# Kernel tuning notes

Hardware: AMD Instinct MI355X
Metric: run time of the kernel (lower is better)

The kernel has to match this reference:

```python
import jax, jax.numpy as jnp
import numpy as np

B, S, H, DH = 4, 1024, 8, 64
D = H * DH
CLIP_K = 5
NUM_RPR = 2 * CLIP_K + 1  # 11


def setup_inputs() -> dict:
    key = jax.random.key(0)
    ks = jax.random.split(key, 12)
    w_scale = 0.01  # truncated_normal stddev approx
    inp = {
        'q': jax.random.normal(ks[0], (B, S, D), jnp.float32),
        'k': jax.random.normal(ks[1], (B, S, D), jnp.float32),
        'v': jax.random.normal(ks[2], (B, S, D), jnp.float32),
        'rpr_matrix': jax.random.randint(ks[3], (S, S), 0, NUM_RPR, jnp.int32),
        'wq_kernel': jax.random.normal(ks[4], (D, D), jnp.float32) * w_scale,
        'wq_bias': jnp.zeros((D,), jnp.float32),
        'wk_kernel': jax.random.normal(ks[5], (D, D), jnp.float32) * w_scale,
        'wk_bias': jnp.zeros((D,), jnp.float32),
        'wv_kernel': jax.random.normal(ks[6], (D, D), jnp.float32) * w_scale,
        'wv_bias': jnp.zeros((D,), jnp.float32),
        'krpr': jax.random.normal(ks[7], (NUM_RPR, DH), jnp.float32),
    }
    return inp


def reference(q, k, v, rpr_matrix, wq_kernel, wq_bias, wk_kernel, wk_bias,
              wv_kernel, wv_bias, krpr):
    b, s, d = q.shape
    dh = krpr.shape[-1]
    h = d // dh

    def proj(x, w, bias):
        # [B,S,D] -> [B,H,S,DH]
        y = x.reshape(-1, d) @ w + bias
        return y.reshape(b, s, h, dh).transpose(0, 2, 1, 3)

    qh = proj(q, wq_kernel, wq_bias)
    kh = proj(k, wk_kernel, wk_bias)
    vh = proj(v, wv_kernel, wv_bias)

    # standard QK^T scores
    scores = jnp.einsum('bhqd,bhkd->bhqk', qh, kh)
    # RPR key bias: gather per-relative-position key embeddings (note: original
    # code uses krpr for BOTH the key-side and value-side RPR; vrpr is unused)
    alpha = krpr[rpr_matrix]  # [Sq, Sk, DH]
    scores = scores + jnp.einsum('bhqd,qkd->bhqk', qh, alpha)
    scores = scores / jnp.sqrt(jnp.float32(dh))

    probs = jax.nn.softmax(scores, axis=-1)

    ctx = jnp.einsum('bhqk,bhkd->bhqd', probs, vh)
    ctx = ctx + jnp.einsum('bhqk,qkd->bhqd', probs, alpha)

    # [B,H,S,DH] -> [B,S,D]
    return ctx.transpose(0, 2, 1, 3).reshape(b, s, d)
```

## Files before the change

### kernel.cpp

```cpp
#include <hip/hip_runtime.h>

typedef unsigned short u16;
typedef unsigned int u32;
typedef __attribute__((ext_vector_type(8))) short short8;
typedef __attribute__((ext_vector_type(4))) float f32x4;
typedef _Float16 f16x2 __attribute__((ext_vector_type(2)));

__device__ __forceinline__ float bf2f(u16 v) {
  return __uint_as_float(((u32)v) << 16);
}
__device__ __forceinline__ u16 f2bf(float f) {
  u32 u = __float_as_uint(f);
  return (u16)((u + 0x7fffu + ((u >> 16) & 1u)) >> 16);
}
__device__ __forceinline__ u32 pk2(float lo, float hi) {
  return (u32)f2bf(lo) | ((u32)f2bf(hi) << 16);
}

__device__ __forceinline__ float ld1in(const void* p, size_t i, bool f32) {
  return f32 ? ((const float*)p)[i] : bf2f(((const u16*)p)[i]);
}
__device__ __forceinline__ float4 ld4in(const void* p, size_t i, bool f32) {
  if (f32) return *(const float4*)((const float*)p + i);
  ushort4 u = *(const ushort4*)((const u16*)p + i);
  return make_float4(bf2f(u.x), bf2f(u.y), bf2f(u.z), bf2f(u.w));
}

__device__ __forceinline__ uint4 ld8ws_pk(const u16* p, size_t i) {
  return *(const uint4*)(p + i);
}


__global__ void rpr_detect_kernel(const u16* __restrict__ q, int* __restrict__ flag) {
  __shared__ int cnt4[4];
  int t = threadIdx.x, c = 0;
  for (int i = t; i < 8192; i += 256) {
    unsigned e = (q[i] >> 7) & 0xff;
    c += (e >= 0xC0) ? 1 : 0;
  }
#pragma unroll
  for (int off = 1; off < 64; off <<= 1) c += __shfl_xor(c, off);
  if ((t & 63) == 0) cnt4[t >> 6] = c;
  __syncthreads();
  if (t == 0) *flag = (cnt4[0] + cnt4[1] + cnt4[2] + cnt4[3] > 128) ? 1 : 0;
}

template <typename WT>
__global__ __launch_bounds__(256, 2) void rpr_proj_mfma(
    const void* __restrict__ xq, const void* __restrict__ xk, const void* __restrict__ xv,
    const void* __restrict__ wqp, const void* __restrict__ wkp, const void* __restrict__ wvp,
    const void* __restrict__ bqp, const void* __restrict__ bkp, const void* __restrict__ bvp,
    WT* __restrict__ ws, const int* __restrict__ flagp) {
  const bool f32 = (*flagp != 0);
  const int z = blockIdx.z;
  const void* __restrict__ X = (z == 0) ? xq : (z == 1) ? xk : xv;
  const void* __restrict__ W = (z == 0) ? wqp : (z == 1) ? wkp : wvp;
  const void* __restrict__ Bb = (z == 0) ? bqp : (z == 1) ? bkp : bvp;
  WT* __restrict__ O = ws + (size_t)z * (4096u * 512u);

  __shared__ u32 as32[2][64][20];
  __shared__ u32 bs32[2][64][20];

  const int t = threadIdx.x;
  const int wvi = t >> 6, lane = t & 63;
  const int quad = lane >> 4, col = lane & 15;
  const int m0 = blockIdx.y * 64, n0 = blockIdx.x * 64;
  const int am = t >> 2, akc = t & 3;
  const int bkx = t & 15, bnx = (t >> 4) * 4;

  f32x4 acc[4] = {{0.f, 0.f, 0.f, 0.f}, {0.f, 0.f, 0.f, 0.f},
                  {0.f, 0.f, 0.f, 0.f}, {0.f, 0.f, 0.f, 0.f}};

  auto loadA = [&](int k0, uint4& ra) {
    if (!f32) {
      ra = *(const uint4*)((const u16*)X + (size_t)(m0 + am) * 512 + k0 + akc * 8);
    } else {
      const float* xf = (const float*)X + (size_t)(m0 + am) * 512 + k0 + akc * 8;
      float4 a = *(const float4*)xf, b = *(const float4*)(xf + 4);
      ra.x = pk2(a.x, a.y); ra.y = pk2(a.z, a.w);
      ra.z = pk2(b.x, b.y); ra.w = pk2(b.z, b.w);
    }
  };
  auto loadB = [&](int k0, uint4& rb) {
    if (!f32) {
      const u16* w0 = (const u16*)W + (size_t)(k0 + 2 * bkx) * 512 + n0 + bnx;
      ushort4 r0 = *(const ushort4*)w0;
      ushort4 r1 = *(const ushort4*)(w0 + 512);
      rb.x = (u32)r0.x | ((u32)r1.x << 16);
      rb.y = (u32)r0.y | ((u32)r1.y << 16);
      rb.z = (u32)r0.z | ((u32)r1.z << 16);
      rb.w = (u32)r0.w | ((u32)r1.w << 16);
    } else {
      float4 r0 = ld4in(W, (size_t)(k0 + 2 * bkx) * 512 + n0 + bnx, true);
      float4 r1 = ld4in(W, (size_t)(k0 + 2 * bkx + 1) * 512 + n0 + bnx, true);
      rb.x = pk2(r0.x, r1.x);
      rb.y = pk2(r0.y, r1.y);
      rb.z = pk2(r0.z, r1.z);
      rb.w = pk2(r0.w, r1.w);
    }
  };

  {
    uint4 ra, rb;
    loadA(0, ra);
    loadB(0, rb);
    *(uint4*)&as32[0][am][akc * 4] = ra;
    bs32[0][bnx + 0][bkx] = rb.x;
    bs32[0][bnx + 1][bkx] = rb.y;
    bs32[0][bnx + 2][bkx] = rb.z;
    bs32[0][bnx + 3][bkx] = rb.w;
  }
  __syncthreads();

  for (int it = 0; it < 16; ++it) {
    const int cur = it & 1;
    uint4 ra, rb;
    if (it < 15) {
      loadA((it + 1) * 32, ra);
      loadB((it + 1) * 32, rb);
    }
    short8 aF = *(const short8*)((const u16*)&as32[cur][wvi * 16 + col][0] + quad * 8);
#pragma unroll
    for (int c = 0; c < 4; ++c) {
      short8 bF = *(const short8*)((const u16*)&bs32[cur][c * 16 + col][0] + quad * 8);
      acc[c] = __builtin_amdgcn_mfma_f32_16x16x32_bf16(aF, bF, acc[c], 0, 0, 0);
    }
    if (it < 15) {
      *(uint4*)&as32[1 - cur][am][akc * 4] = ra;
      bs32[1 - cur][bnx + 0][bkx] = rb.x;
      bs32[1 - cur][bnx + 1][bkx] = rb.y;
      bs32[1 - cur][bnx + 2][bkx] = rb.z;
      bs32[1 - cur][bnx + 3][bkx] = rb.w;
    }
    __syncthreads();
  }

  const int h = blockIdx.x;
#pragma unroll
  for (int c = 0; c < 4; ++c) {
    float bias = ld1in(Bb, (size_t)(n0 + c * 16 + col), f32);
#pragma unroll
    for (int reg = 0; reg < 4; ++reg) {
      int m = m0 + wvi * 16 + quad * 4 + reg;
      int bb = m >> 10, s = m & 1023;
      O[((size_t)((bb * 8 + h) * 1024 + s)) * 64 + c * 16 + col] =
          f2bf(acc[c][reg] + bias);
    }
  }
}

template <typename WT>
__global__ __launch_bounds__(256, 2) void rpr_attn_mfma(
    const WT* __restrict__ qkv, const int* __restrict__ rpr,
    const void* __restrict__ krpr, void* __restrict__ out,
    const int* __restrict__ flagp) {
  const bool f32 = (*flagp != 0);
  const int bh = blockIdx.y, q0 = blockIdx.x * 64;
  const int b = bh >> 3, h = bh & 7;
  const WT* __restrict__ qh = qkv + (size_t)bh * 65536;
  const WT* __restrict__ kh = qkv + (size_t)(32 + bh) * 65536;
  const WT* __restrict__ vh = qkv + (size_t)(64 + bh) * 65536;

  __shared__ alignas(16) u16 qps[64][72];
  __shared__ u16 ks[2][64][72];
  __shared__ u32 vs32[2][64][36];
  __shared__ float krl[11][64];
  __shared__ float qrpr[64][12];

  const int t = threadIdx.x;
  const int wvi = t >> 6, lane = t & 63;
  const int quad = lane >> 4, col = lane & 15;
  const int sr = t >> 2, sc4 = (t & 3) * 16;
  const int kp = t & 31, dg = (t >> 5) * 8;
  const int swk = (((t & 3) + sr) & 3) * 16;
  const int fo0 = ((quad + 2 * (col & 3)) & 7) * 8;
  const int fo1 = fo0 ^ 32;
  const int vq = kp >> 2, vr = kp & 3;

  u16* __restrict__ psw = &qps[0][0] + wvi * (16 * 72);
  const int row0 = wvi * 16 + quad * 4;

  for (int i = t; i < 704; i += 256)
    krl[i >> 6][i & 63] = f32 ? ((const float*)krpr)[i] : bf2f(((const u16*)krpr)[i]);
  {
    size_t base = (size_t)(q0 + sr) * 64 + sc4;
    *(uint4*)&qps[sr][sc4] = ld8ws_pk(qh, base);
    *(uint4*)&qps[sr][sc4 + 8] = ld8ws_pk(qh, base + 8);
  }
  {
    size_t kb = (size_t)sr * 64 + sc4;
    *(uint4*)&ks[0][sr][swk] = ld8ws_pk(kh, kb);
    *(uint4*)&ks[0][sr][swk + 8] = ld8ws_pk(kh, kb + 8);
    size_t vb = (size_t)(2 * kp) * 64 + dg;
    uint4 va = ld8ws_pk(vh, vb), vbb = ld8ws_pk(vh, vb + 64);
    vs32[0][dg + 0][((vq + 0) & 7) * 4 + vr] = (va.x & 0xffffu) | (vbb.x << 16);
    vs32[0][dg + 1][((vq + 2) & 7) * 4 + vr] = (va.x >> 16) | (vbb.x & 0xffff0000u);
    vs32[0][dg + 2][((vq + 4) & 7) * 4 + vr] = (va.y & 0xffffu) | (vbb.y << 16);
    vs32[0][dg + 3][((vq + 6) & 7) * 4 + vr] = (va.y >> 16) | (vbb.y & 0xffff0000u);
    vs32[0][dg + 4][((vq + 0) & 7) * 4 + vr] = (va.z & 0xffffu) | (vbb.z << 16);
    vs32[0][dg + 5][((vq + 2) & 7) * 4 + vr] = (va.z >> 16) | (vbb.z & 0xffff0000u);
    vs32[0][dg + 6][((vq + 4) & 7) * 4 + vr] = (va.w & 0xffffu) | (vbb.w << 16);
    vs32[0][dg + 7][((vq + 6) & 7) * 4 + vr] = (va.w >> 16) | (vbb.w & 0xffff0000u);
  }
  int rid[4][4];
  {
    const int* rbase = rpr + (size_t)(q0 + row0) * 1024 + col;
#pragma unroll
    for (int reg = 0; reg < 4; ++reg)
#pragma unroll
      for (int c = 0; c < 4; ++c) rid[c][reg] = rbase[reg * 1024 + c * 16];
  }
  __syncthreads();
  {
    const float SC = 0.18033688011112042f;
    int r = t >> 2, rb = t & 3;
    float d0 = 0.f, d1 = 0.f, d2 = 0.f;
    for (int d = 0; d < 64; ++d) {
      float qv = bf2f(qps[r][d]);
      d0 = fmaf(qv, krl[rb][d], d0);
      d1 = fmaf(qv, krl[rb + 4][d], d1);
      if (rb < 3) d2 = fmaf(qv, krl[rb + 8][d], d2);
    }
    qrpr[r][rb] = d0 * SC;
    qrpr[r][rb + 4] = d1 * SC;
    if (rb < 3) qrpr[r][rb + 8] = d2 * SC;
  }
  short8 qA0, qA1;
  {
    const u16* qrow = &qps[wvi * 16 + col][0];
    qA0 = *(const short8*)(qrow + quad * 8);
    qA1 = *(const short8*)(qrow + 32 + quad * 8);
  }
  __syncthreads();

  float bins[4][11] = {};
  f32x4 ctx[4] = {{0.f, 0.f, 0.f, 0.f}, {0.f, 0.f, 0.f, 0.f},
                  {0.f, 0.f, 0.f, 0.f}, {0.f, 0.f, 0.f, 0.f}};

  for (int kt = 0; kt < 16; ++kt) {
    const int cur = kt & 1;
    uint4 pk0, pk1, pva, pvb;
    int ridn[4][4];
    if (kt < 15) {
      size_t kb = (size_t)((kt + 1) * 64 + sr) * 64 + sc4;
      pk0 = ld8ws_pk(kh, kb);
      pk1 = ld8ws_pk(kh, kb + 8);
      size_t vb = (size_t)((kt + 1) * 64 + 2 * kp) * 64 + dg;
      pva = ld8ws_pk(vh, vb);
      pvb = ld8ws_pk(vh, vb + 64);
      const int* rbase = rpr + (size_t)(q0 + row0) * 1024 + (kt + 1) * 64 + col;
#pragma unroll
      for (int reg = 0; reg < 4; ++reg)
#pragma unroll
        for (int c = 0; c < 4; ++c) ridn[c][reg] = rbase[reg * 1024 + c * 16];
    }
    f32x4 sc[4];
#pragma unroll
    for (int c = 0; c < 4; ++c) {
      const u16* kb = &ks[cur][c * 16 + col][0];
      short8 kB0 = *(const short8*)(kb + fo0);
      short8 kB1 = *(const short8*)(kb + fo1);
      f32x4 a = {0.f, 0.f, 0.f, 0.f};
      a = __builtin_amdgcn_mfma_f32_16x16x32_bf16(qA0, kB0, a, 0, 0, 0);
      a = __builtin_amdgcn_mfma_f32_16x16x32_bf16(qA1, kB1, a, 0, 0, 0);
      sc[c] = a;
    }
#pragma unroll
    for (int reg = 0; reg < 4; ++reg) {
      const int row = row0 + reg;
      float p4[4];
#pragma unroll
      for (int c = 0; c < 4; ++c) {
        float x = fmaf(sc[c][reg], 0.18033688011112042f, qrpr[row][rid[c][reg]]);
        float pe;
        asm("v_exp_f32 %0, %1" : "=v"(pe) : "v"(x));
        p4[c] = pe;
      }
      f16x2 ph01 = __builtin_bit_cast(f16x2, __builtin_amdgcn_cvt_pkrtz(p4[0], p4[1]));
      f16x2 ph23 = __builtin_bit_cast(f16x2, __builtin_amdgcn_cvt_pkrtz(p4[2], p4[3]));
      u32 m01 = (1u << (u32)rid[0][reg]) | (0x10000u << (u32)rid[1][reg]);
      u32 m23 = (1u << (u32)rid[2][reg]) | (0x10000u << (u32)rid[3][reg]);
#pragma unroll
      for (int r = 0; r < 11; ++r) {
        u32 s01 = ((m01 >> r) & 0x00010001u) * 0x3C00u;
        u32 s23 = ((m23 >> r) & 0x00010001u) * 0x3C00u;
        bins[reg][r] = __builtin_amdgcn_fdot2(ph01, __builtin_bit_cast(f16x2, s01),
                                              bins[reg][r], false);
        bins[reg][r] = __builtin_amdgcn_fdot2(ph23, __builtin_bit_cast(f16x2, s23),
                                              bins[reg][r], false);
      }
      u32 plo, phi;
      asm("v_cvt_pk_bf16_f32 %0, %1, %2" : "=v"(plo) : "v"(p4[0]), "v"(p4[1]));
      asm("v_cvt_pk_bf16_f32 %0, %1, %2" : "=v"(phi) : "v"(p4[2]), "v"(p4[3]));
      *(uint2*)(psw + (quad * 4 + reg) * 72 + col * 4) = make_uint2(plo, phi);
    }

    short8 pA0, pA1;
    {
      const u16* prow = psw + col * 72;
      pA0 = *(const short8*)(prow + quad * 8);
      pA1 = *(const short8*)(prow + 32 + quad * 8);
    }
#pragma unroll
    for (int c = 0; c < 4; ++c) {
      const u16* vrow = (const u16*)&vs32[cur][c * 16 + col][0];
      short8 vB0 = *(const short8*)(vrow + fo0);
      short8 vB1 = *(const short8*)(vrow + fo1);
      ctx[c] = __builtin_amdgcn_mfma_f32_16x16x32_bf16(pA0, vB0, ctx[c], 0, 0, 0);
      ctx[c] = __builtin_amdgcn_mfma_f32_16x16x32_bf16(pA1, vB1, ctx[c], 0, 0, 0);
    }
    if (kt < 15) {
      *(uint4*)&ks[1 - cur][sr][swk] = pk0;
      *(uint4*)&ks[1 - cur][sr][swk + 8] = pk1;
      vs32[1 - cur][dg + 0][((vq + 0) & 7) * 4 + vr] = (pva.x & 0xffffu) | (pvb.x << 16);
      vs32[1 - cur][dg + 1][((vq + 2) & 7) * 4 + vr] = (pva.x >> 16) | (pvb.x & 0xffff0000u);
      vs32[1 - cur][dg + 2][((vq + 4) & 7) * 4 + vr] = (pva.y & 0xffffu) | (pvb.y << 16);
      vs32[1 - cur][dg + 3][((vq + 6) & 7) * 4 + vr] = (pva.y >> 16) | (pvb.y & 0xffff0000u);
      vs32[1 - cur][dg + 4][((vq + 0) & 7) * 4 + vr] = (pva.z & 0xffffu) | (pvb.z << 16);
      vs32[1 - cur][dg + 5][((vq + 2) & 7) * 4 + vr] = (pva.z >> 16) | (pvb.z & 0xffff0000u);
      vs32[1 - cur][dg + 6][((vq + 4) & 7) * 4 + vr] = (pva.w & 0xffffu) | (pvb.w << 16);
      vs32[1 - cur][dg + 7][((vq + 6) & 7) * 4 + vr] = (pva.w >> 16) | (pvb.w & 0xffff0000u);
#pragma unroll
      for (int reg = 0; reg < 4; ++reg)
#pragma unroll
        for (int c = 0; c < 4; ++c) rid[c][reg] = ridn[c][reg];
    }
    __syncthreads();
  }

#pragma unroll
  for (int off = 1; off < 16; off <<= 1) {
#pragma unroll
    for (int reg = 0; reg < 4; ++reg) {
#pragma unroll
      for (int r = 0; r < 11; ++r) bins[reg][r] += __shfl_xor(bins[reg][r], off);
    }
  }
#pragma unroll
  for (int reg = 0; reg < 4; ++reg) {
    int row = wvi * 16 + quad * 4 + reg;
    float l = bins[reg][0];
#pragma unroll
    for (int r = 1; r < 11; ++r) l += bins[reg][r];
    float inv = 1.f / l;
#pragma unroll
    for (int c = 0; c < 4; ++c) {
      float v = ctx[c][reg];
#pragma unroll
      for (int r = 0; r < 11; ++r) v = fmaf(bins[reg][r], krl[r][c * 16 + col], v);
      size_t oidx = (size_t)(b * 1024 + q0 + row) * 512 + h * 64 + c * 16 + col;
      if (f32) ((float*)out)[oidx] = v * inv;
      else ((u16*)out)[oidx] = f2bf(v * inv);
    }
  }
}

extern "C" void kernel_launch(void* const* d_in, const int* in_sizes, int n_in,
                              void* d_out, int out_size, void* d_ws, size_t ws_size,
                              hipStream_t stream) {
  const void* q = d_in[0];
  const void* k = d_in[1];
  const void* v = d_in[2];
  const int* rpr = (const int*)d_in[3];
  const void* wq = d_in[4];
  const void* bq = d_in[5];
  const void* wk = d_in[6];
  const void* bk = d_in[7];
  const void* wv = d_in[8];
  const void* bv = d_in[9];
  const void* krpr = d_in[10];

  int* flag = (int*)d_ws;
  u16* ws = (u16*)((char*)d_ws + 1024);

  rpr_detect_kernel<<<1, 256, 0, stream>>>((const u16*)q, flag);
  rpr_proj_mfma<u16><<<dim3(8, 64, 3), 256, 0, stream>>>(
      q, k, v, wq, wk, wv, bq, bk, bv, ws, flag);
  rpr_attn_mfma<u16><<<dim3(16, 32), 256, 0, stream>>>(
      ws, rpr, krpr, d_out, flag);
}
```

Baseline: 183.0 us.

## Split attention key range across two blocks and merge partials in separate kernel

The attention kernel gains a PARTIAL mode that processes half of the key tiles per block (grid z=2), writing unnormalized context and per-RPR bin sums to workspace. A new merge kernel sums the two halves, applies the krpr bin correction and normalizes. This doubles the block count from 512 to 1024 to improve occupancy across the GPU's CUs, at the cost of extra fp32 partial traffic and an additional launch. The rpr index prefetch is also changed from a register double-buffer to a same-iteration load. The split path runs only if the workspace is large enough.

Result: slower. 218.1 us (+19.2%).

```diff
diff --git a/kernel.cpp b/kernel.cpp
--- a/kernel.cpp
+++ b/kernel.cpp
@@ -149,17 +149,21 @@
   }
 }
 
-template <typename WT>
+template <int PARTIAL>
 __global__ __launch_bounds__(256, 2) void rpr_attn_mfma(
-    const WT* __restrict__ qkv, const int* __restrict__ rpr,
+    const u16* __restrict__ qkv, const int* __restrict__ rpr,
     const void* __restrict__ krpr, void* __restrict__ out,
-    const int* __restrict__ flagp) {
+    const int* __restrict__ flagp, float* __restrict__ pctx,
+    float* __restrict__ pbins) {
   const bool f32 = (*flagp != 0);
   const int bh = blockIdx.y, q0 = blockIdx.x * 64;
   const int b = bh >> 3, h = bh & 7;
-  const WT* __restrict__ qh = qkv + (size_t)bh * 65536;
-  const WT* __restrict__ kh = qkv + (size_t)(32 + bh) * 65536;
-  const WT* __restrict__ vh = qkv + (size_t)(64 + bh) * 65536;
+  const int half = PARTIAL ? blockIdx.z : 0;
+  const int kt0 = half * 8;
+  const int NT = PARTIAL ? 8 : 16;
+  const u16* __restrict__ qh = qkv + (size_t)bh * 65536;
+  const u16* __restrict__ kh = qkv + (size_t)(32 + bh) * 65536;
+  const u16* __restrict__ vh = qkv + (size_t)(64 + bh) * 65536;
 
   __shared__ alignas(16) u16 qps[64][72];
   __shared__ u16 ks[2][64][72];
@@ -188,10 +192,10 @@
     *(uint4*)&qps[sr][sc4 + 8] = ld8ws_pk(qh, base + 8);
   }
   {
-    size_t kb = (size_t)sr * 64 + sc4;
+    size_t kb = (size_t)(kt0 * 64 + sr) * 64 + sc4;
     *(uint4*)&ks[0][sr][swk] = ld8ws_pk(kh, kb);
     *(uint4*)&ks[0][sr][swk + 8] = ld8ws_pk(kh, kb + 8);
-    size_t vb = (size_t)(2 * kp) * 64 + dg;
+    size_t vb = (size_t)(kt0 * 64 + 2 * kp) * 64 + dg;
     uint4 va = ld8ws_pk(vh, vb), vbb = ld8ws_pk(vh, vb + 64);
     vs32[0][dg + 0][((vq + 0) & 7) * 4 + vr] = (va.x & 0xffffu) | (vbb.x << 16);
     vs32[0][dg + 1][((vq + 2) & 7) * 4 + vr] = (va.x >> 16) | (vbb.x & 0xffff0000u);
@@ -201,14 +205,6 @@
     vs32[0][dg + 5][((vq + 2) & 7) * 4 + vr] = (va.z >> 16) | (vbb.z & 0xffff0000u);
     vs32[0][dg + 6][((vq + 4) & 7) * 4 + vr] = (va.w & 0xffffu) | (vbb.w << 16);
     vs32[0][dg + 7][((vq + 6) & 7) * 4 + vr] = (va.w >> 16) | (vbb.w & 0xffff0000u);
-  }
-  int rid[4][4];
-  {
-    const int* rbase = rpr + (size_t)(q0 + row0) * 1024 + col;
-#pragma unroll
-    for (int reg = 0; reg < 4; ++reg)
-#pragma unroll
-      for (int c = 0; c < 4; ++c) rid[c][reg] = rbase[reg * 1024 + c * 16];
   }
   __syncthreads();
   {
@@ -237,22 +233,25 @@
   f32x4 ctx[4] = {{0.f, 0.f, 0.f, 0.f}, {0.f, 0.f, 0.f, 0.f},
                   {0.f, 0.f, 0.f, 0.f}, {0.f, 0.f, 0.f, 0.f}};
 
-  for (int kt = 0; kt < 16; ++kt) {
-    const int cur = kt & 1;
+  for (int i = 0; i < NT; ++i) {
+    const int kt = kt0 + i;
+    const int cur = i & 1;
     uint4 pk0, pk1, pva, pvb;
-    int ridn[4][4];
-    if (kt < 15) {
+    if (i < NT - 1) {
       size_t kb = (size_t)((kt + 1) * 64 + sr) * 64 + sc4;
       pk0 = ld8ws_pk(kh, kb);
       pk1 = ld8ws_pk(kh, kb + 8);
       size_t vb = (size_t)((kt + 1) * 64 + 2 * kp) * 64 + dg;
       pva = ld8ws_pk(vh, vb);
       pvb = ld8ws_pk(vh, vb + 64);
-      const int* rbase = rpr + (size_t)(q0 + row0) * 1024 + (kt + 1) * 64 + col;
+    }
+    int rid[4][4];
+    {
+      const int* rbase = rpr + (size_t)(q0 + row0) * 1024 + kt * 64 + col;
 #pragma unroll
       for (int reg = 0; reg < 4; ++reg)
 #pragma unroll
-        for (int c = 0; c < 4; ++c) ridn[c][reg] = rbase[reg * 1024 + c * 16];
+        for (int c = 0; c < 4; ++c) rid[c][reg] = rbase[reg * 1024 + c * 16];
     }
     f32x4 sc[4];
 #pragma unroll
@@ -309,7 +308,7 @@
       ctx[c] = __builtin_amdgcn_mfma_f32_16x16x32_bf16(pA0, vB0, ctx[c], 0, 0, 0);
       ctx[c] = __builtin_amdgcn_mfma_f32_16x16x32_bf16(pA1, vB1, ctx[c], 0, 0, 0);
     }
-    if (kt < 15) {
+    if (i < NT - 1) {
       *(uint4*)&ks[1 - cur][sr][swk] = pk0;
       *(uint4*)&ks[1 - cur][sr][swk + 8] = pk1;
       vs32[1 - cur][dg + 0][((vq + 0) & 7) * 4 + vr] = (pva.x & 0xffffu) | (pvb.x << 16);
@@ -320,10 +319,6 @@
       vs32[1 - cur][dg + 5][((vq + 2) & 7) * 4 + vr] = (pva.z >> 16) | (pvb.z & 0xffff0000u);
       vs32[1 - cur][dg + 6][((vq + 4) & 7) * 4 + vr] = (pva.w & 0xffffu) | (pvb.w << 16);
       vs32[1 - cur][dg + 7][((vq + 6) & 7) * 4 + vr] = (pva.w >> 16) | (pvb.w & 0xffff0000u);
-#pragma unroll
-      for (int reg = 0; reg < 4; ++reg)
-#pragma unroll
-        for (int c = 0; c < 4; ++c) rid[c][reg] = ridn[c][reg];
     }
     __syncthreads();
   }
@@ -336,9 +331,27 @@
       for (int r = 0; r < 11; ++r) bins[reg][r] += __shfl_xor(bins[reg][r], off);
     }
   }
+
+  if (PARTIAL) {
+    const size_t blk = (size_t)((half * 16 + blockIdx.x) * 32 + bh);
+    float* cp = pctx + blk * 4096;
+    float* bp = pbins + blk * 768;
+#pragma unroll
+    for (int reg = 0; reg < 4; ++reg) {
+      int row = row0 + reg;
+#pragma unroll
+      for (int c = 0; c < 4; ++c) cp[(size_t)row * 64 + c * 16 + col] = ctx[c][reg];
+      if (col == 0) {
+#pragma unroll
+        for (int r = 0; r < 11; ++r) bp[row * 12 + r] = bins[reg][r];
+      }
+    }
+    return;
+  }
+
 #pragma unroll
   for (int reg = 0; reg < 4; ++reg) {
-    int row = wvi * 16 + quad * 4 + reg;
+    int row = row0 + reg;
     float l = bins[reg][0];
 #pragma unroll
     for (int r = 1; r < 11; ++r) l += bins[reg][r];
@@ -352,6 +365,47 @@
       if (f32) ((float*)out)[oidx] = v * inv;
       else ((u16*)out)[oidx] = f2bf(v * inv);
     }
+  }
+}
+
+__global__ __launch_bounds__(256) void rpr_attn_merge(
+    const float* __restrict__ pctx, const float* __restrict__ pbins,
+    const void* __restrict__ krpr, void* __restrict__ out,
+    const int* __restrict__ flagp) {
+  const bool f32 = (*flagp != 0);
+  const int qx = blockIdx.x, bh = blockIdx.y;
+  const int b = bh >> 3, h = bh & 7;
+  __shared__ float krl[11][64];
+  const int t = threadIdx.x;
+  for (int i = t; i < 704; i += 256)
+    krl[i >> 6][i & 63] = f32 ? ((const float*)krpr)[i] : bf2f(((const u16*)krpr)[i]);
+  __syncthreads();
+
+  const int row = t >> 2, dq = (t & 3) * 16;
+  const size_t blk0 = (size_t)(qx * 32 + bh);
+  const size_t blk1 = blk0 + 512;
+  const float* c0 = pctx + blk0 * 4096 + (size_t)row * 64;
+  const float* c1 = pctx + blk1 * 4096 + (size_t)row * 64;
+  const float* b0 = pbins + blk0 * 768 + row * 12;
+  const float* b1 = pbins + blk1 * 768 + row * 12;
+
+  float bt[11];
+  float l = 0.f;
+#pragma unroll
+  for (int r = 0; r < 11; ++r) {
+    bt[r] = b0[r] + b1[r];
+    l += bt[r];
+  }
+  float inv = 1.f / l;
+  size_t obase = (size_t)(b * 1024 + qx * 64 + row) * 512 + h * 64;
+#pragma unroll
+  for (int j = 0; j < 16; ++j) {
+    int d = dq + j;
+    float v = c0[d] + c1[d];
+#pragma unroll
+    for (int r = 0; r < 11; ++r) v = fmaf(bt[r], krl[r][d], v);
+    if (f32) ((float*)out)[obase + d] = v * inv;
+    else ((u16*)out)[obase + d] = f2bf(v * inv);
   }
 }
 
@@ -372,10 +426,21 @@
 
   int* flag = (int*)d_ws;
   u16* ws = (u16*)((char*)d_ws + 1024);
+  const size_t QKV_BYTES = 3ull * 4096 * 512 * 2;
+  float* pctx = (float*)((char*)d_ws + 1024 + QKV_BYTES);
+  float* pbins = pctx + 1024ull * 4096;
+  const size_t NEED = 1024 + QKV_BYTES + 1024ull * 4096 * 4 + 1024ull * 768 * 4;
 
   rpr_detect_kernel<<<1, 256, 0, stream>>>((const u16*)q, flag);
   rpr_proj_mfma<u16><<<dim3(8, 64, 3), 256, 0, stream>>>(
       q, k, v, wq, wk, wv, bq, bk, bv, ws, flag);
-  rpr_attn_mfma<u16><<<dim3(16, 32), 256, 0, stream>>>(
-      ws, rpr, krpr, d_out, flag);
-}
+  if (ws_size >= NEED) {
+    rpr_attn_mfma<1><<<dim3(16, 32, 2), 256, 0, stream>>>(
+        ws, rpr, krpr, d_out, flag, pctx, pbins);
+    rpr_attn_merge<<<dim3(16, 32), 256, 0, stream>>>(
+        pctx, pbins, krpr, d_out, flag);
+  } else {
+    rpr_attn_mfma<0><<<dim3(16, 32), 256, 0, stream>>>(
+        ws, rpr, krpr, d_out, flag, nullptr, nullptr);
+  }
+}
```
